# Performance work log

Hardware: AMD Instinct MI355X
Metric: run time of the kernel (lower is better)

## Reference

```python
import jax, jax.numpy as jnp
import numpy as np

D = 192      # model dim (out_channels)
DIN = 384    # d_inner = 2*D
N = 16       # d_state
DTR = 12     # dt_rank = ceil(D/16)
K = 4        # depthwise conv kernel size
NB = 3       # total mamba blocks (2 stacked + 1 in downsample)


def setup_inputs() -> dict:
    key = jax.random.key(0)
    ks = jax.random.split(key, 8)
    rn = lambda k, shape, s: jax.random.normal(k, shape, jnp.float32) * s
    inp = {
        "x": jax.random.normal(ks[0], (2, 96, 56, 56), jnp.float32),
        "proj_w": rn(ks[1], (D, 96), 0.1),
        "proj_b": jnp.zeros((D,), jnp.float32),
        "bn_g": jnp.ones((D,), jnp.float32),
        "bn_b": jnp.zeros((D,), jnp.float32),
        "bn_mean": jnp.zeros((D,), jnp.float32),
        "bn_var": jnp.ones((D,), jnp.float32),
        "ln_g": jnp.ones((NB, D), jnp.float32),
        "ln_b": jnp.zeros((NB, D), jnp.float32),
        "Win": rn(ks[2], (NB, 2 * DIN, D), 0.05),
        "b_in": jnp.zeros((NB, 2 * DIN), jnp.float32),
        "conv_w": rn(ks[3], (NB, DIN, K), 0.2),
        "conv_b": jnp.zeros((NB, DIN), jnp.float32),
        "Wx": rn(ks[4], (NB, DTR + 2 * N, DIN), 0.05),
        "Wdt": rn(ks[5], (NB, DIN, DTR), 0.05),
        "bdt": jnp.full((NB, DIN), -4.6, jnp.float32),  # softplus ~ 0.01
        "A_log": jnp.log(jnp.broadcast_to(jnp.arange(1, N + 1, dtype=jnp.float32), (NB, DIN, N))),
        "Dskip": jnp.ones((NB, DIN), jnp.float32),
        "Wout": rn(ks[6], (NB, D, DIN), 0.05),
        "bout": jnp.zeros((NB, D), jnp.float32),
    }
    return inp


def _mamba(x, ln_g, ln_b, Win, b_in, conv_w, conv_b, Wx, Wdt, bdt, A_log, Dskip, Wout, bout):
    # x: (B, C, H, W) -> flatten spatial dims to a sequence (B, L, C)
    B, C, H, W = x.shape
    L = H * W
    seq = x.reshape(B, C, L).transpose(0, 2, 1)
    mu = seq.mean(-1, keepdims=True)
    var = seq.var(-1, keepdims=True)
    h = (seq - mu) * jax.lax.rsqrt(var + 1e-5) * ln_g + ln_b  # LayerNorm
    xz = jnp.einsum('bld,ed->ble', h, Win) + b_in              # (B, L, 2*DIN)
    xi, z = jnp.split(xz, 2, axis=-1)
    # depthwise causal conv1d along L
    xc = jnp.pad(xi.transpose(0, 2, 1), ((0, 0), (0, 0), (K - 1, 0)))
    xc = jax.lax.conv_general_dilated(xc, conv_w[:, None, :], (1,), 'VALID',
                                      feature_group_count=DIN) + conv_b[:, None]
    xi = jax.nn.silu(xc).transpose(0, 2, 1)                    # (B, L, DIN)
    proj = jnp.einsum('ble,pe->blp', xi, Wx)                   # (B, L, DTR+2N)
    dtl = proj[..., :DTR]
    Bm = proj[..., DTR:DTR + N]
    Cm = proj[..., DTR + N:]
    dt = jax.nn.softplus(jnp.einsum('blr,er->ble', dtl, Wdt) + bdt)  # (B, L, DIN)
    A = -jnp.exp(A_log)                                         # (DIN, N)
    dA = jnp.exp(dt[..., None] * A)                             # (B, L, DIN, N)
    dBx = (dt * xi)[..., None] * Bm[:, :, None, :]              # (B, L, DIN, N)

    def step(hc, t):
        dA_t, dBx_t, C_t = t
        hc = dA_t * hc + dBx_t                                  # (B, DIN, N)
        return hc, jnp.einsum('ben,bn->be', hc, C_t)

    h0 = jnp.zeros((B, DIN, N), x.dtype)
    _, ys = jax.lax.scan(step, h0, (dA.transpose(1, 0, 2, 3),
                                    dBx.transpose(1, 0, 2, 3),
                                    Cm.transpose(1, 0, 2)))
    y = ys.transpose(1, 0, 2) + Dskip * xi
    y = y * jax.nn.silu(z)
    out = jnp.einsum('ble,de->bld', y, Wout) + bout
    return out.transpose(0, 2, 1).reshape(B, C, H, W)


def _maxpool2(x):
    return jax.lax.reduce_window(x, -jnp.inf, jax.lax.max,
                                 (1, 1, 2, 2), (1, 1, 2, 2), 'VALID')


def reference(x, proj_w, proj_b, bn_g, bn_b, bn_mean, bn_var, ln_g, ln_b, Win, b_in,
              conv_w, conv_b, Wx, Wdt, bdt, A_log, Dskip, Wout, bout):
    # proj (conv1x1) + BatchNorm (eval-mode running stats)
    x = jnp.einsum('bchw,oc->bohw', x, proj_w) + proj_b[:, None, None]
    x = (x - bn_mean[:, None, None]) * jax.lax.rsqrt(bn_var[:, None, None] + 1e-5) \
        * bn_g[:, None, None] + bn_b[:, None, None]
    blk = lambda i, v: _mamba(v, ln_g[i], ln_b[i], Win[i], b_in[i], conv_w[i], conv_b[i],
                              Wx[i], Wdt[i], bdt[i], A_log[i], Dskip[i], Wout[i], bout[i])
    for i in range(2):  # residual mamba blocks
        x = x + blk(i, x)
    skip = x
    x = blk(2, _maxpool2(x))  # downsample: maxpool then mamba (no residual)
    return (x, skip)
```

## Files before the change

kernel.cpp:

```cpp
#include <hip/hip_runtime.h>

typedef __attribute__((ext_vector_type(8))) __bf16 bf16x8;
typedef __attribute__((ext_vector_type(4))) __bf16 bf16x4;
typedef __attribute__((ext_vector_type(4))) float f32x4;

#define DEV static __device__ __forceinline__

DEV float fast_rcp(float x) { return __builtin_amdgcn_rcpf(x); }
DEV float sigm(float x) { return fast_rcp(1.f + __expf(-x)); }
DEV float siluf(float x) { return x * sigm(x); }
DEV float softplusf(float x) { return x > 20.f ? x : __logf(1.f + __expf(x)); }

__global__ __launch_bounds__(256) void k_proj_wcvt(
    const float* __restrict__ x, const float* __restrict__ pw,
    const float* __restrict__ pb, const float* __restrict__ bng,
    const float* __restrict__ bnb, const float* __restrict__ bnm,
    const float* __restrict__ bnv, float* __restrict__ v,
    const float* __restrict__ Win, const float* __restrict__ Wout,
    const float* __restrict__ Wx, __bf16* __restrict__ Wb)
{
  constexpr int SAP = 104;
  __shared__ __bf16 As[64 * SAP];
  __shared__ __bf16 Ws[64 * SAP];
  const int tid = threadIdx.x;
  const int bid = blockIdx.x;

  if (bid >= 294) {
    const int idx = (bid - 294) * 256 + tid;
    if (idx < 442368) Wb[idx] = (__bf16)Win[idx];
    else if (idx < 663552) Wb[idx] = (__bf16)Wout[idx - 442368];
    else Wb[idx] = (__bf16)Wx[idx - 663552];
    return;
  }

  const int r0 = (bid % 98) * 64;
  const int col0 = (bid / 98) * 64;
  const int b = r0 / 3136, l0 = r0 % 3136;
  const int lane = tid & 63, wv = tid >> 6;
  const int rh = wv >> 1, ch = wv & 1;
  const int lm = lane & 15, quad = lane >> 4;

#pragma unroll
  for (int it = 0; it < 6; ++it) {
    const int idx = tid + it * 256;
    const int c = idx >> 4, l4 = idx & 15;
    const float4 t = *(const float4*)(x + ((size_t)(b * 96 + c)) * 3136 + l0 + l4 * 4);
    As[(l4 * 4 + 0) * SAP + c] = (__bf16)t.x;
    As[(l4 * 4 + 1) * SAP + c] = (__bf16)t.y;
    As[(l4 * 4 + 2) * SAP + c] = (__bf16)t.z;
    As[(l4 * 4 + 3) * SAP + c] = (__bf16)t.w;
  }
#pragma unroll
  for (int it = 0; it < 6; ++it) {
    const int idx = tid + it * 256;
    const int wr = idx / 24, kc = (idx % 24) * 4;
    const float4 t = *(const float4*)(pw + (size_t)(col0 + wr) * 96 + kc);
    bf16x4 o;
    o[0] = (__bf16)t.x; o[1] = (__bf16)t.y; o[2] = (__bf16)t.z; o[3] = (__bf16)t.w;
    *(bf16x4*)(&Ws[wr * SAP + kc]) = o;
  }
  __syncthreads();

  f32x4 acc[2][2] = {};
#pragma unroll
  for (int ks = 0; ks < 3; ++ks) {
    const int kb = ks * 32 + quad * 8;
    bf16x8 a0 = *(const bf16x8*)(&As[(rh * 32 + lm) * SAP + kb]);
    bf16x8 a1 = *(const bf16x8*)(&As[(rh * 32 + 16 + lm) * SAP + kb]);
    bf16x8 b0 = *(const bf16x8*)(&Ws[(ch * 32 + lm) * SAP + kb]);
    bf16x8 b1 = *(const bf16x8*)(&Ws[(ch * 32 + 16 + lm) * SAP + kb]);
    acc[0][0] = __builtin_amdgcn_mfma_f32_16x16x32_bf16(a0, b0, acc[0][0], 0, 0, 0);
    acc[0][1] = __builtin_amdgcn_mfma_f32_16x16x32_bf16(a0, b1, acc[0][1], 0, 0, 0);
    acc[1][0] = __builtin_amdgcn_mfma_f32_16x16x32_bf16(a1, b0, acc[1][0], 0, 0, 0);
    acc[1][1] = __builtin_amdgcn_mfma_f32_16x16x32_bf16(a1, b1, acc[1][1], 0, 0, 0);
  }

#pragma unroll
  for (int ti = 0; ti < 2; ++ti)
#pragma unroll
    for (int tj = 0; tj < 2; ++tj) {
      const int gcol = col0 + ch * 32 + tj * 16 + lm;
      const float s = rsqrtf(bnv[gcol] + 1e-5f) * bng[gcol];
      const float sh = (pb[gcol] - bnm[gcol]) * s + bnb[gcol];
#pragma unroll
      for (int j = 0; j < 4; ++j) {
        const int grow = r0 + rh * 32 + ti * 16 + quad * 4 + j;
        v[(size_t)grow * 192 + gcol] = acc[ti][tj][j] * s + sh;
      }
    }
}

__global__ __launch_bounds__(256) void k_conv(
    const float* __restrict__ xz, __bf16* __restrict__ xiB,
    const float* __restrict__ cw, const float* __restrict__ cb,
    int Lseq, int nthreads)
{
  const int idx = blockIdx.x * 256 + threadIdx.x;
  if (idx >= nthreads) return;
  const int e = idx % 384;
  const int seg = idx / 384;
  const int nseg = Lseq / 8;
  const int b = seg / nseg;
  const int l0 = (seg % nseg) * 8;
  const float4 w4 = *(const float4*)(cw + e * 4);
  const float bv = cb[e];
  float xv[11];
#pragma unroll
  for (int k = 0; k < 11; ++k) {
    const int l = l0 - 3 + k;
    xv[k] = (l >= 0) ? xz[(size_t)(b * Lseq + l) * 768 + e] : 0.f;
  }
#pragma unroll
  for (int j = 0; j < 8; ++j) {
    const float a = bv + xv[j] * w4.x + xv[j + 1] * w4.y + xv[j + 2] * w4.z + xv[j + 3] * w4.w;
    xiB[(size_t)(b * Lseq + l0 + j) * 384 + e] = (__bf16)siluf(a);
  }
}

constexpr int EPI_XZ = 0, EPI_G2 = 1, EPI_RES = 2, EPI_RES_SKIP = 3, EPI_OUT2 = 4;

template <int AMODE, int NT, int EPI>
__global__ __launch_bounds__(256) void k_gemm(
    const void* __restrict__ Ain, const __bf16* __restrict__ W,
    const float* __restrict__ bias, float* __restrict__ O,
    int M, int K, int Nvalid,
    float* __restrict__ dtlbuf, float* __restrict__ bcbuf,
    float* __restrict__ oflt,
    const float* __restrict__ lng, const float* __restrict__ lnb,
    int Lseq)
{
  constexpr int SA = 200;
  constexpr int CT = (NT == 1) ? 2 : 4;
  __shared__ __bf16 As[64 * SA];
  __shared__ __bf16 Ws[64 * NT * SA];
  __shared__ float lnS[(AMODE >= 2) ? 384 : 1];
  const int tid = threadIdx.x;
  const int r0 = blockIdx.x * 64;
  const int col0 = blockIdx.y * (64 * NT);
  const int lane = tid & 63, wv = tid >> 6;
  const int rh = (NT == 1) ? (wv >> 1) : (wv & 1);
  const int ch = (NT == 1) ? (wv & 1) : (wv >> 1);
  const int lm = lane & 15, quad = lane >> 4;

  if constexpr (AMODE >= 2) {
    if (tid < 192) { lnS[tid] = lng[tid]; lnS[192 + tid] = lnb[tid]; }
    __syncthreads();
  }

  f32x4 acc[2][CT] = {};
  const int nkp = K / 192;
  for (int kp = 0; kp < nkp; ++kp) {
    if (kp) __syncthreads();
    if constexpr (AMODE == 1) {
      const __bf16* Ab = (const __bf16*)Ain;
#pragma unroll
      for (int it = 0; it < 6; ++it) {
        const int idx = tid + it * 256;
        const int row = idx / 24, kc = (idx % 24) * 8;
        const int gr = min(r0 + row, M - 1);
        bf16x8 val = *(const bf16x8*)(Ab + (size_t)gr * K + kp * 192 + kc);
        *(bf16x8*)(&As[row * SA + kc]) = val;
      }
    } else {
      const float* A = (const float*)Ain;
      const int row = tid >> 2, part = tid & 3;
      const int gr = min(r0 + row, M - 1);
      const int cbase = part * 48;
      float4 tv[12];
      if constexpr (AMODE == 2) {
#pragma unroll
        for (int j = 0; j < 12; ++j)
          tv[j] = *(const float4*)(A + (size_t)gr * 192 + cbase + j * 4);
      } else {
        const int bb = gr / 784, l2 = gr % 784;
        const int h2 = l2 / 28, w2 = l2 % 28;
        const float* p0 = A + (size_t)(bb * 3136 + h2 * 112 + w2 * 2) * 192;
#pragma unroll
        for (int j = 0; j < 12; ++j) {
          const int cc = cbase + j * 4;
          const float4 a0 = *(const float4*)(p0 + cc);
          const float4 a1 = *(const float4*)(p0 + 192 + cc);
          const float4 a2 = *(const float4*)(p0 + 56 * 192 + cc);
          const float4 a3 = *(const float4*)(p0 + 57 * 192 + cc);
          tv[j].x = fmaxf(fmaxf(a0.x, a1.x), fmaxf(a2.x, a3.x));
          tv[j].y = fmaxf(fmaxf(a0.y, a1.y), fmaxf(a2.y, a3.y));
          tv[j].z = fmaxf(fmaxf(a0.z, a1.z), fmaxf(a2.z, a3.z));
          tv[j].w = fmaxf(fmaxf(a0.w, a1.w), fmaxf(a2.w, a3.w));
        }
      }
      float s = 0.f, sq = 0.f;
#pragma unroll
      for (int j = 0; j < 12; ++j) {
        s += tv[j].x + tv[j].y + tv[j].z + tv[j].w;
        sq += tv[j].x * tv[j].x + tv[j].y * tv[j].y + tv[j].z * tv[j].z + tv[j].w * tv[j].w;
      }
      s += __shfl_xor(s, 1); s += __shfl_xor(s, 2);
      sq += __shfl_xor(sq, 1); sq += __shfl_xor(sq, 2);
      const float mean = s * (1.f / 192.f);
      const float rstd = rsqrtf(sq * (1.f / 192.f) - mean * mean + 1e-5f);
#pragma unroll
      for (int j = 0; j < 12; ++j) {
        const int c = cbase + j * 4;
        bf16x4 o;
        o[0] = (__bf16)((tv[j].x - mean) * rstd * lnS[c + 0] + lnS[192 + c + 0]);
        o[1] = (__bf16)((tv[j].y - mean) * rstd * lnS[c + 1] + lnS[192 + c + 1]);
        o[2] = (__bf16)((tv[j].z - mean) * rstd * lnS[c + 2] + lnS[192 + c + 2]);
        o[3] = (__bf16)((tv[j].w - mean) * rstd * lnS[c + 3] + lnS[192 + c + 3]);
        *(bf16x4*)(&As[row * SA + c]) = o;
      }
    }
#pragma unroll
    for (int it = 0; it < 6 * NT; ++it) {
      const int idx = tid + it * 256;
      const int wr = idx / 24, kc = (idx % 24) * 8;
      const int gw = col0 + wr;
      bf16x8 val = {};
      if (gw < Nvalid) val = *(const bf16x8*)(W + (size_t)gw * K + kp * 192 + kc);
      *(bf16x8*)(&Ws[wr * SA + kc]) = val;
    }
    __syncthreads();
#pragma unroll
    for (int ks = 0; ks < 6; ++ks) {
      const int kb = ks * 32 + quad * 8;
      bf16x8 a0 = *(const bf16x8*)(&As[(rh * 32 + lm) * SA + kb]);
      bf16x8 a1 = *(const bf16x8*)(&As[(rh * 32 + 16 + lm) * SA + kb]);
#pragma unroll
      for (int tj = 0; tj < CT; ++tj) {
        bf16x8 bfr = *(const bf16x8*)(&Ws[(ch * (16 * CT) + tj * 16 + lm) * SA + kb]);
        acc[0][tj] = __builtin_amdgcn_mfma_f32_16x16x32_bf16(a0, bfr, acc[0][tj], 0, 0, 0);
        acc[1][tj] = __builtin_amdgcn_mfma_f32_16x16x32_bf16(a1, bfr, acc[1][tj], 0, 0, 0);
      }
    }
  }

  if constexpr (EPI == EPI_G2) {
    __shared__ float dtlS[64 * 12];
#pragma unroll
    for (int ti = 0; ti < 2; ++ti)
#pragma unroll
      for (int tj = 0; tj < CT; ++tj) {
        const int colt = ch * (16 * CT) + tj * 16 + lm;
#pragma unroll
        for (int j = 0; j < 4; ++j) {
          const int rowt = rh * 32 + ti * 16 + quad * 4 + j;
          const int grow = r0 + rowt;
          const float val = acc[ti][tj][j];
          if (colt < 12) dtlS[rowt * 12 + colt] = val;
          else if (colt < 44 && grow < M)
            bcbuf[(size_t)grow * 32 + (colt - 12)] = val;
        }
      }
    __syncthreads();
    for (int idx = tid; idx < 64 * 12; idx += 256) {
      const int grow = r0 + idx / 12;
      if (grow < M) dtlbuf[(size_t)grow * 12 + idx % 12] = dtlS[idx];
    }
  } else {
#pragma unroll
    for (int ti = 0; ti < 2; ++ti)
#pragma unroll
      for (int tj = 0; tj < CT; ++tj) {
        const int colt = ch * (16 * CT) + tj * 16 + lm;
        const int gcol = col0 + colt;
        const float bv = bias[gcol];
#pragma unroll
        for (int j = 0; j < 4; ++j) {
          const int rowt = rh * 32 + ti * 16 + quad * 4 + j;
          const int grow = r0 + rowt;
          if (grow >= M) continue;
          const float val = acc[ti][tj][j] + bv;
          if constexpr (EPI == EPI_XZ) {
            O[(size_t)grow * 768 + gcol] = val;
          } else if constexpr (EPI == EPI_RES) {
            O[(size_t)grow * 192 + gcol] += val;
          } else if constexpr (EPI == EPI_RES_SKIP) {
            const float nv = O[(size_t)grow * 192 + gcol] + val;
            O[(size_t)grow * 192 + gcol] = nv;
            const int b = grow / 3136, l = grow % 3136;
            oflt[b * 602112 + gcol * 3136 + l] = nv;
          } else {
            const int b = grow / 784, l = grow % 784;
            oflt[b * 150528 + gcol * 784 + l] = val;
          }
        }
      }
  }
}

constexpr int SC_LC = 28, SC_T = 7, SC_TN = 4;

DEV void compute_dts(const float* __restrict__ dtl, const float* __restrict__ Wdt,
                     const float* __restrict__ bdt, int rowbase, int e, int t,
                     float* dtlS, float* wdtS)
{
  for (int idx = t; idx < SC_LC * 12; idx += 128)
    dtlS[idx] = dtl[(size_t)(rowbase + idx / 12) * 12 + idx % 12];
#pragma unroll
  for (int r = 0; r < 12; ++r) wdtS[r * 128 + t] = Wdt[(size_t)e * 12 + r];
}

__global__ __launch_bounds__(128) void k_scan1(
    const float* __restrict__ dtl, const __bf16* __restrict__ xi,
    const float* __restrict__ bc, const float* __restrict__ Wdt,
    const float* __restrict__ bdt, const float* __restrict__ A_log,
    float* __restrict__ P, float* __restrict__ S, int Lseq, int NC)
{
  __shared__ float Bs[SC_LC * 16];
  __shared__ float dts[SC_LC * 128];
  __shared__ float dtlS[SC_LC * 12];
  __shared__ float wdtS[12 * 128];
  const int t = threadIdx.x;
  const int e = blockIdx.y * 128 + t;
  const int c = blockIdx.x % NC;
  const int b = blockIdx.x / NC;
  const int rowbase = b * Lseq + c * SC_LC;

  for (int idx = t; idx < SC_LC * 16; idx += 128) {
    const int l = idx >> 4, q = idx & 15;
    Bs[idx] = bc[(size_t)(rowbase + l) * 32 + q];
  }
  compute_dts(dtl, Wdt, bdt, rowbase, e, t, dtlS, wdtS);
  const float bdte = bdt[e];

  float An2[16];
  {
    const float4* a4 = (const float4*)(A_log + e * 16);
    float4 t0 = a4[0], t1 = a4[1], t2 = a4[2], t3 = a4[3];
    float tmp[16] = {t0.x, t0.y, t0.z, t0.w, t1.x, t1.y, t1.z, t1.w,
                     t2.x, t2.y, t2.z, t2.w, t3.x, t3.y, t3.z, t3.w};
#pragma unroll
    for (int n = 0; n < 16; ++n) An2[n] = -__expf(tmp[n]) * 1.44269504f;
  }
  __syncthreads();
  for (int l = 0; l < SC_LC; ++l) {
    float a = bdte;
#pragma unroll
    for (int r = 0; r < 12; ++r) a += dtlS[l * 12 + r] * wdtS[r * 128 + t];
    dts[l * 128 + t] = softplusf(a);
  }

  float h[16], ap[16];
#pragma unroll
  for (int n = 0; n < 16; ++n) { h[n] = 0.f; ap[n] = 1.f; }

  float xA[SC_T], xB[SC_T];
  auto LOADA = [&](int tt) {
#pragma unroll
    for (int j = 0; j < SC_T; ++j)
      xA[j] = (float)xi[(size_t)(rowbase + tt * SC_T + j) * 384 + e];
  };
  auto LOADB = [&](int tt) {
#pragma unroll
    for (int j = 0; j < SC_T; ++j)
      xB[j] = (float)xi[(size_t)(rowbase + tt * SC_T + j) * 384 + e];
  };
  auto COMP = [&](const float (&x8)[SC_T], int tt) {
#pragma unroll
    for (int j = 0; j < SC_T; ++j) {
      const int l = tt * SC_T + j;
      const float dtv = dts[l * 128 + t];
      const float u = dtv * x8[j];
      const float* Brow = &Bs[l * 16];
#pragma unroll
      for (int n = 0; n < 16; ++n) {
        const float a = __builtin_amdgcn_exp2f(dtv * An2[n]);
        h[n] = a * h[n] + u * Brow[n];
        ap[n] *= a;
      }
    }
  };

  LOADA(0);
#pragma unroll
  for (int tt = 0; tt < SC_TN; ++tt) {
    if (tt & 1) { if (tt + 1 < SC_TN) LOADA(tt + 1); COMP(xB, tt); }
    else        { if (tt + 1 < SC_TN) LOADB(tt + 1); COMP(xA, tt); }
  }

  const size_t o = ((size_t)(b * NC + c) * 384 + e) * 16;
#pragma unroll
  for (int q = 0; q < 4; ++q) {
    *(float4*)(P + o + q * 4) = make_float4(ap[q*4], ap[q*4+1], ap[q*4+2], ap[q*4+3]);
    *(float4*)(S + o + q * 4) = make_float4(h[q*4], h[q*4+1], h[q*4+2], h[q*4+3]);
  }
}

__global__ __launch_bounds__(256) void k_carry(
    const float* __restrict__ P, float* __restrict__ SH, int NC)
{
  const int tid = blockIdx.x * 256 + threadIdx.x;
  const int b = tid / 6144, r = tid % 6144;
  size_t o = (size_t)b * NC * 6144 + r;
  float h = 0.f;
  for (int c0 = 0; c0 < NC; c0 += 4) {
    float p[4], s[4];
#pragma unroll
    for (int k = 0; k < 4; ++k) { p[k] = P[o + (size_t)k * 6144]; s[k] = SH[o + (size_t)k * 6144]; }
#pragma unroll
    for (int k = 0; k < 4; ++k) { SH[o + (size_t)k * 6144] = h; h = p[k] * h + s[k]; }
    o += (size_t)4 * 6144;
  }
}

__global__ __launch_bounds__(128) void k_scan2(
    const float* __restrict__ dtl, const __bf16* __restrict__ xi,
    const float* __restrict__ bc, const float* __restrict__ xz,
    const float* __restrict__ Wdt, const float* __restrict__ bdt,
    const float* __restrict__ A_log, const float* __restrict__ Dskip,
    const float* __restrict__ H0, __bf16* __restrict__ y, int Lseq, int NC)
{
  __shared__ float BCs[SC_LC * 32];
  __shared__ float dts[SC_LC * 128];
  __shared__ float dtlS[SC_LC * 12];
  __shared__ float wdtS[12 * 128];
  const int t = threadIdx.x;
  const int e = blockIdx.y * 128 + t;
  const int c = blockIdx.x % NC;
  const int b = blockIdx.x / NC;
  const int rowbase = b * Lseq + c * SC_LC;

  for (int idx = t; idx < SC_LC * 32; idx += 128)
    BCs[idx] = bc[(size_t)rowbase * 32 + idx];
  compute_dts(dtl, Wdt, bdt, rowbase, e, t, dtlS, wdtS);
  const float bdte = bdt[e];

  float An2[16];
  {
    const float4* a4 = (const float4*)(A_log + e * 16);
    float4 t0 = a4[0], t1 = a4[1], t2 = a4[2], t3 = a4[3];
    float tmp[16] = {t0.x, t0.y, t0.z, t0.w, t1.x, t1.y, t1.z, t1.w,
                     t2.x, t2.y, t2.z, t2.w, t3.x, t3.y, t3.z, t3.w};
#pragma unroll
    for (int n = 0; n < 16; ++n) An2[n] = -__expf(tmp[n]) * 1.44269504f;
  }
  float h[16];
  {
    const size_t o = ((size_t)(b * NC + c) * 384 + e) * 16;
    const float4* h4 = (const float4*)(H0 + o);
    float4 t0 = h4[0], t1 = h4[1], t2 = h4[2], t3 = h4[3];
    h[0]=t0.x; h[1]=t0.y; h[2]=t0.z; h[3]=t0.w;
    h[4]=t1.x; h[5]=t1.y; h[6]=t1.z; h[7]=t1.w;
    h[8]=t2.x; h[9]=t2.y; h[10]=t2.z; h[11]=t2.w;
    h[12]=t3.x; h[13]=t3.y; h[14]=t3.z; h[15]=t3.w;
  }
  __syncthreads();
  for (int l = 0; l < SC_LC; ++l) {
    float a = bdte;
#pragma unroll
    for (int r = 0; r < 12; ++r) a += dtlS[l * 12 + r] * wdtS[r * 128 + t];
    dts[l * 128 + t] = softplusf(a);
  }
  const float Dse = Dskip[e];

  float xA[SC_T], zA[SC_T], xB[SC_T], zB[SC_T];
  auto LOADA = [&](int tt) {
#pragma unroll
    for (int j = 0; j < SC_T; ++j) {
      const size_t r = (size_t)(rowbase + tt * SC_T + j);
      xA[j] = (float)xi[r * 384 + e];
      zA[j] = xz[r * 768 + 384 + e];
    }
  };
  auto LOADB = [&](int tt) {
#pragma unroll
    for (int j = 0; j < SC_T; ++j) {
      const size_t r = (size_t)(rowbase + tt * SC_T + j);
      xB[j] = (float)xi[r * 384 + e];
      zB[j] = xz[r * 768 + 384 + e];
    }
  };
  auto COMP = [&](const float (&x8)[SC_T], const float (&z8)[SC_T], int tt) {
#pragma unroll
    for (int j = 0; j < SC_T; ++j) {
      const int l = tt * SC_T + j;
      const float dtv = dts[l * 128 + t];
      const float xiv = x8[j];
      const float u = dtv * xiv;
      const float* Brow = &BCs[l * 32];
      const float* Crow = Brow + 16;
      float yv = 0.f;
#pragma unroll
      for (int n = 0; n < 16; ++n) {
        const float a = __builtin_amdgcn_exp2f(dtv * An2[n]);
        h[n] = a * h[n] + u * Brow[n];
        yv += h[n] * Crow[n];
      }
      y[(size_t)(rowbase + l) * 384 + e] = (__bf16)((yv + Dse * xiv) * siluf(z8[j]));
    }
  };

  LOADA(0);
#pragma unroll
  for (int tt = 0; tt < SC_TN; ++tt) {
    if (tt & 1) { if (tt + 1 < SC_TN) LOADA(tt + 1); COMP(xB, zB, tt); }
    else        { if (tt + 1 < SC_TN) LOADB(tt + 1); COMP(xA, zA, tt); }
  }
}

extern "C" void kernel_launch(void* const* d_in, const int* in_sizes, int n_in,
                              void* d_out, int out_size, void* d_ws, size_t ws_size,
                              hipStream_t stream)
{
  const float* x    = (const float*)d_in[0];
  const float* pw   = (const float*)d_in[1];
  const float* pb   = (const float*)d_in[2];
  const float* bng  = (const float*)d_in[3];
  const float* bnb  = (const float*)d_in[4];
  const float* bnm  = (const float*)d_in[5];
  const float* bnv  = (const float*)d_in[6];
  const float* lng  = (const float*)d_in[7];
  const float* lnb  = (const float*)d_in[8];
  const float* Win  = (const float*)d_in[9];
  const float* b_in = (const float*)d_in[10];
  const float* cw   = (const float*)d_in[11];
  const float* cb   = (const float*)d_in[12];
  const float* Wx   = (const float*)d_in[13];
  const float* Wdt  = (const float*)d_in[14];
  const float* bdt  = (const float*)d_in[15];
  const float* Alog = (const float*)d_in[16];
  const float* Dsk  = (const float*)d_in[17];
  const float* Wout = (const float*)d_in[18];
  const float* bout = (const float*)d_in[19];

  float* wsf = (float*)d_ws;
  float* v    = wsf;
  float* xz   = v + 1204224;
  float* dtlb = xz + 4816896;
  float* bcb  = dtlb + 75264;
  float* Sb   = bcb + 200704;
  __bf16* xiB = (__bf16*)(Sb + 1376256);
  __bf16* yB  = (__bf16*)(Sb + 1376256 + 1204224);
  __bf16* Wb  = (__bf16*)(Sb + 1376256 + 2408448);

  float* out0 = (float*)d_out;
  float* out1 = out0 + 301056;
  float* Pbig = out0;
  float* Psml = xz + 2408448;

  k_proj_wcvt<<<3084, 256, 0, stream>>>(x, pw, pb, bng, bnb, bnm, bnv, v,
                                        Win, Wout, Wx, Wb);

  for (int i = 0; i < 3; ++i) {
    const int big = (i < 2) ? 1 : 0;
    const int Lseq = big ? 3136 : 784;
    const int M = 2 * Lseq;
    const int NC = Lseq / SC_LC;
    const int MB = (M + 63) / 64;
    const float* lng_i = lng + i * 192;
    const float* lnb_i = lnb + i * 192;
    const float* bin_i = b_in + i * 768;
    const float* cw_i  = cw + i * 384 * 4;
    const float* cb_i  = cb + i * 384;
    const float* Wdt_i = Wdt + i * 384 * 12;
    const float* bdt_i = bdt + i * 384;
    const float* Al_i  = Alog + i * 384 * 16;
    const float* Ds_i  = Dsk + i * 384;
    const float* bo_i  = bout + i * 192;
    const __bf16* Winb_i  = Wb + i * 147456;
    const __bf16* Woutb_i = Wb + 442368 + i * 73728;
    const __bf16* Wxb_i   = Wb + 663552 + i * 16896;
    float* Pb = big ? Pbig : Psml;

    if (big)
      k_gemm<2, 2, EPI_XZ><<<dim3(MB, 6), 256, 0, stream>>>(
          v, Winb_i, bin_i, xz, M, 192, 768,
          nullptr, nullptr, nullptr, lng_i, lnb_i, Lseq);
    else
      k_gemm<3, 2, EPI_XZ><<<dim3(MB, 6), 256, 0, stream>>>(
          v, Winb_i, bin_i, xz, M, 192, 768,
          nullptr, nullptr, nullptr, lng_i, lnb_i, Lseq);
    k_conv<<<(M * 384 / 8 + 255) / 256, 256, 0, stream>>>(
        xz, xiB, cw_i, cb_i, Lseq, M * 384 / 8);
    k_gemm<1, 1, EPI_G2><<<dim3(MB, 1), 256, 0, stream>>>(
        xiB, Wxb_i, nullptr, nullptr, M, 384, 44,
        dtlb, bcb, nullptr, nullptr, nullptr, Lseq);
    k_scan1<<<dim3(2 * NC, 3), 128, 0, stream>>>(
        dtlb, xiB, bcb, Wdt_i, bdt_i, Al_i, Pb, Sb, Lseq, NC);
    k_carry<<<48, 256, 0, stream>>>(Pb, Sb, NC);
    k_scan2<<<dim3(2 * NC, 3), 128, 0, stream>>>(
        dtlb, xiB, bcb, xz, Wdt_i, bdt_i, Al_i, Ds_i, Sb, yB, Lseq, NC);
    if (i == 0)
      k_gemm<1, 1, EPI_RES><<<dim3(MB, 3), 256, 0, stream>>>(
          yB, Woutb_i, bo_i, v, M, 384, 192,
          nullptr, nullptr, nullptr, nullptr, nullptr, Lseq);
    else if (i == 1)
      k_gemm<1, 1, EPI_RES_SKIP><<<dim3(MB, 3), 256, 0, stream>>>(
          yB, Woutb_i, bo_i, v, M, 384, 192,
          nullptr, nullptr, out1, nullptr, nullptr, Lseq);
    else
      k_gemm<1, 1, EPI_OUT2><<<dim3(MB, 3), 256, 0, stream>>>(
          yB, Woutb_i, bo_i, v, M, 384, 192,
          nullptr, nullptr, out0, nullptr, nullptr, Lseq);
  }
}
```

Baseline: 394.1 us.

## Fuse causal depthwise conv and SiLU into in-projection GEMM epilogue

Removes the separate conv kernel. The in-projection GEMM now applies the depthwise causal conv and SiLU in its epilogue for the xi half and writes bf16 xi directly, while the z half goes to a compact 384-wide buffer. A 3-row halo is normalized and recomputed per block with a scalar dot product, which avoids writing and reading back the full fp32 xz tensor. The cost is extra LDS use, a redundant halo GEMM and extra syncs in the GEMM blocks. Some leftover no-op code appears in the conv loop.

```diff
diff --git a/kernel.cpp b/kernel.cpp
--- a/kernel.cpp
+++ b/kernel.cpp
@@ -90,33 +90,6 @@
     }
 }
 
-__global__ __launch_bounds__(256) void k_conv(
-    const float* __restrict__ xz, __bf16* __restrict__ xiB,
-    const float* __restrict__ cw, const float* __restrict__ cb,
-    int Lseq, int nthreads)
-{
-  const int idx = blockIdx.x * 256 + threadIdx.x;
-  if (idx >= nthreads) return;
-  const int e = idx % 384;
-  const int seg = idx / 384;
-  const int nseg = Lseq / 8;
-  const int b = seg / nseg;
-  const int l0 = (seg % nseg) * 8;
-  const float4 w4 = *(const float4*)(cw + e * 4);
-  const float bv = cb[e];
-  float xv[11];
-#pragma unroll
-  for (int k = 0; k < 11; ++k) {
-    const int l = l0 - 3 + k;
-    xv[k] = (l >= 0) ? xz[(size_t)(b * Lseq + l) * 768 + e] : 0.f;
-  }
-#pragma unroll
-  for (int j = 0; j < 8; ++j) {
-    const float a = bv + xv[j] * w4.x + xv[j + 1] * w4.y + xv[j + 2] * w4.z + xv[j + 3] * w4.w;
-    xiB[(size_t)(b * Lseq + l0 + j) * 384 + e] = (__bf16)siluf(a);
-  }
-}
-
 constexpr int EPI_XZ = 0, EPI_G2 = 1, EPI_RES = 2, EPI_RES_SKIP = 3, EPI_OUT2 = 4;
 
 template <int AMODE, int NT, int EPI>
@@ -127,12 +100,15 @@
     float* __restrict__ dtlbuf, float* __restrict__ bcbuf,
     float* __restrict__ oflt,
     const float* __restrict__ lng, const float* __restrict__ lnb,
+    const float* __restrict__ cw, const float* __restrict__ cb,
+    __bf16* __restrict__ xiBout, float* __restrict__ zb,
     int Lseq)
 {
   constexpr int SA = 200;
   constexpr int CT = (NT == 1) ? 2 : 4;
   __shared__ __bf16 As[64 * SA];
   __shared__ __bf16 Ws[64 * NT * SA];
+  __shared__ __bf16 As2[(EPI == EPI_XZ) ? 3 * SA : 1];
   __shared__ float lnS[(AMODE >= 2) ? 384 : 1];
   const int tid = threadIdx.x;
   const int r0 = blockIdx.x * 64;
@@ -163,50 +139,58 @@
       }
     } else {
       const float* A = (const float*)Ain;
-      const int row = tid >> 2, part = tid & 3;
-      const int gr = min(r0 + row, M - 1);
-      const int cbase = part * 48;
-      float4 tv[12];
-      if constexpr (AMODE == 2) {
-#pragma unroll
-        for (int j = 0; j < 12; ++j)
-          tv[j] = *(const float4*)(A + (size_t)gr * 192 + cbase + j * 4);
-      } else {
-        const int bb = gr / 784, l2 = gr % 784;
-        const int h2 = l2 / 28, w2 = l2 % 28;
-        const float* p0 = A + (size_t)(bb * 3136 + h2 * 112 + w2 * 2) * 192;
+      const int nwork = (EPI == EPI_XZ && col0 < 384) ? 2 : 1;
+      for (int w = 0; w < nwork; ++w) {
+        int row, part, gr;
+        __bf16* dst;
+        if (w == 0) { row = tid >> 2; part = tid & 3; gr = min(r0 + row, M - 1); dst = &As[row * SA]; }
+        else {
+          if (tid >= 12) break;
+          row = tid >> 2; part = tid & 3; gr = max(r0 - 3 + row, 0); dst = &As2[row * SA];
+        }
+        const int cbase = part * 48;
+        float4 tv[12];
+        if constexpr (AMODE == 2) {
+#pragma unroll
+          for (int j = 0; j < 12; ++j)
+            tv[j] = *(const float4*)(A + (size_t)gr * 192 + cbase + j * 4);
+        } else {
+          const int bb = gr / 784, l2 = gr % 784;
+          const int h2 = l2 / 28, w2 = l2 % 28;
+          const float* p0 = A + (size_t)(bb * 3136 + h2 * 112 + w2 * 2) * 192;
+#pragma unroll
+          for (int j = 0; j < 12; ++j) {
+            const int cc = cbase + j * 4;
+            const float4 a0 = *(const float4*)(p0 + cc);
+            const float4 a1 = *(const float4*)(p0 + 192 + cc);
+            const float4 a2 = *(const float4*)(p0 + 56 * 192 + cc);
+            const float4 a3 = *(const float4*)(p0 + 57 * 192 + cc);
+            tv[j].x = fmaxf(fmaxf(a0.x, a1.x), fmaxf(a2.x, a3.x));
+            tv[j].y = fmaxf(fmaxf(a0.y, a1.y), fmaxf(a2.y, a3.y));
+            tv[j].z = fmaxf(fmaxf(a0.z, a1.z), fmaxf(a2.z, a3.z));
+            tv[j].w = fmaxf(fmaxf(a0.w, a1.w), fmaxf(a2.w, a3.w));
+          }
+        }
+        float s = 0.f, sq = 0.f;
 #pragma unroll
         for (int j = 0; j < 12; ++j) {
-          const int cc = cbase + j * 4;
-          const float4 a0 = *(const float4*)(p0 + cc);
-          const float4 a1 = *(const float4*)(p0 + 192 + cc);
-          const float4 a2 = *(const float4*)(p0 + 56 * 192 + cc);
-          const float4 a3 = *(const float4*)(p0 + 57 * 192 + cc);
-          tv[j].x = fmaxf(fmaxf(a0.x, a1.x), fmaxf(a2.x, a3.x));
-          tv[j].y = fmaxf(fmaxf(a0.y, a1.y), fmaxf(a2.y, a3.y));
-          tv[j].z = fmaxf(fmaxf(a0.z, a1.z), fmaxf(a2.z, a3.z));
-          tv[j].w = fmaxf(fmaxf(a0.w, a1.w), fmaxf(a2.w, a3.w));
-        }
-      }
-      float s = 0.f, sq = 0.f;
-#pragma unroll
-      for (int j = 0; j < 12; ++j) {
-        s += tv[j].x + tv[j].y + tv[j].z + tv[j].w;
-        sq += tv[j].x * tv[j].x + tv[j].y * tv[j].y + tv[j].z * tv[j].z + tv[j].w * tv[j].w;
-      }
-      s += __shfl_xor(s, 1); s += __shfl_xor(s, 2);
-      sq += __shfl_xor(sq, 1); sq += __shfl_xor(sq, 2);
-      const float mean = s * (1.f / 192.f);
-      const float rstd = rsqrtf(sq * (1.f / 192.f) - mean * mean + 1e-5f);
-#pragma unroll
-      for (int j = 0; j < 12; ++j) {
-        const int c = cbase + j * 4;
-        bf16x4 o;
-        o[0] = (__bf16)((tv[j].x - mean) * rstd * lnS[c + 0] + lnS[192 + c + 0]);
-        o[1] = (__bf16)((tv[j].y - mean) * rstd * lnS[c + 1] + lnS[192 + c + 1]);
-        o[2] = (__bf16)((tv[j].z - mean) * rstd * lnS[c + 2] + lnS[192 + c + 2]);
-        o[3] = (__bf16)((tv[j].w - mean) * rstd * lnS[c + 3] + lnS[192 + c + 3]);
-        *(bf16x4*)(&As[row * SA + c]) = o;
+          s += tv[j].x + tv[j].y + tv[j].z + tv[j].w;
+          sq += tv[j].x * tv[j].x + tv[j].y * tv[j].y + tv[j].z * tv[j].z + tv[j].w * tv[j].w;
+        }
+        s += __shfl_xor(s, 1); s += __shfl_xor(s, 2);
+        sq += __shfl_xor(sq, 1); sq += __shfl_xor(sq, 2);
+        const float mean = s * (1.f / 192.f);
+        const float rstd = rsqrtf(sq * (1.f / 192.f) - mean * mean + 1e-5f);
+#pragma unroll
+        for (int j = 0; j < 12; ++j) {
+          const int c = cbase + j * 4;
+          bf16x4 o;
+          o[0] = (__bf16)((tv[j].x - mean) * rstd * lnS[c + 0] + lnS[192 + c + 0]);
+          o[1] = (__bf16)((tv[j].y - mean) * rstd * lnS[c + 1] + lnS[192 + c + 1]);
+          o[2] = (__bf16)((tv[j].z - mean) * rstd * lnS[c + 2] + lnS[192 + c + 2]);
+          o[3] = (__bf16)((tv[j].w - mean) * rstd * lnS[c + 3] + lnS[192 + c + 3]);
+          *(bf16x4*)(dst + c) = o;
+        }
       }
     }
 #pragma unroll
@@ -233,7 +217,98 @@
     }
   }
 
-  if constexpr (EPI == EPI_G2) {
+  if constexpr (EPI == EPI_XZ) {
+    if (col0 < 384) {
+      __syncthreads();
+      float bval[2] = {0.f, 0.f};
+#pragma unroll
+      for (int jj = 0; jj < 2; ++jj) {
+        const int j = tid + jj * 256;
+        if (j < 384) {
+          const int row3 = j >> 7, col = j & 127;
+          float a = bias[col0 + col];
+#pragma unroll
+          for (int kk = 0; kk < 24; ++kk) {
+            const bf16x8 a8 = *(const bf16x8*)(&As2[row3 * SA + kk * 8]);
+            const bf16x8 w8 = *(const bf16x8*)(&Ws[col * SA + kk * 8]);
+#pragma unroll
+            for (int q = 0; q < 8; ++q) a += (float)a8[q] * (float)w8[q];
+          }
+          bval[jj] = a;
+        }
+      }
+      __syncthreads();
+      constexpr int XTP = 132;
+      float* XT = (float*)Ws;
+#pragma unroll
+      for (int jj = 0; jj < 2; ++jj) {
+        const int j = tid + jj * 256;
+        if (j < 384) XT[(j >> 7) * XTP + (j & 127)] = bval[jj];
+      }
+#pragma unroll
+      for (int ti = 0; ti < 2; ++ti)
+#pragma unroll
+        for (int tj = 0; tj < CT; ++tj) {
+          const int colt = ch * (16 * CT) + tj * 16 + lm;
+          const float bv = bias[col0 + colt];
+#pragma unroll
+          for (int j = 0; j < 4; ++j) {
+            const int rowt = rh * 32 + ti * 16 + quad * 4 + j;
+            XT[(rowt + 3) * XTP + colt] = acc[ti][tj][j] + bv;
+          }
+        }
+      __syncthreads();
+      const int c0 = tid & 31;
+      const int rbase = (tid >> 5) * 8;
+#pragma unroll
+      for (int q = 0; q < 4; ++q) {
+        const int col = c0 + 32 * q;
+        const int e = col0 + col;
+        const float4 w4 = *(const float4*)(cw + e * 4);
+        const float cbe = cb[e];
+#pragma unroll
+        for (int rr = 0; rr < 8; ++rr) {
+          const int lrow = rbase + rr;
+          const int lg = r0 + lrow;
+          const int lseq = lg % Lseq;
+          float a = cbe;
+#pragma unroll
+          for (int k = 0; k < 4; ++k) {
+            const float xv = (lseq - 3 + k >= 0) ? XT[(lrow + k) * XTP + col] : 0.f;
+            a += w4[k] * ((const float*)&w4)[k] == 0.f ? 0.f : 0.f;
+            a += 0.f;
+          }
+          a = cbe;
+          if (lseq >= 3) {
+            a += w4.x * XT[(lrow + 0) * XTP + col];
+            a += w4.y * XT[(lrow + 1) * XTP + col];
+            a += w4.z * XT[(lrow + 2) * XTP + col];
+          } else {
+            if (lseq >= 3) a += w4.x * XT[(lrow + 0) * XTP + col];
+            if (lseq >= 2) a += w4.y * XT[(lrow + 1) * XTP + col];
+            if (lseq >= 1) a += w4.z * XT[(lrow + 2) * XTP + col];
+          }
+          a += w4.w * XT[(lrow + 3) * XTP + col];
+          if (lg < M) xiBout[(size_t)lg * 384 + e] = (__bf16)siluf(a);
+        }
+      }
+    } else {
+#pragma unroll
+      for (int ti = 0; ti < 2; ++ti)
+#pragma unroll
+        for (int tj = 0; tj < CT; ++tj) {
+          const int colt = ch * (16 * CT) + tj * 16 + lm;
+          const int gcol = col0 + colt;
+          const float bv = bias[gcol];
+#pragma unroll
+          for (int j = 0; j < 4; ++j) {
+            const int rowt = rh * 32 + ti * 16 + quad * 4 + j;
+            const int grow = r0 + rowt;
+            if (grow < M) zb[(size_t)grow * 384 + (gcol - 384)] = acc[ti][tj][j] + bv;
+          }
+        }
+    }
+  } else if constexpr (EPI == EPI_G2) {
     __shared__ float dtlS[64 * 12];
 #pragma unroll
     for (int ti = 0; ti < 2; ++ti)
@@ -269,9 +344,7 @@
           const int grow = r0 + rowt;
           if (grow >= M) continue;
           const float val = acc[ti][tj][j] + bv;
-          if constexpr (EPI == EPI_XZ) {
-            O[(size_t)grow * 768 + gcol] = val;
-          } else if constexpr (EPI == EPI_RES) {
+          if constexpr (EPI == EPI_RES) {
             O[(size_t)grow * 192 + gcol] += val;
           } else if constexpr (EPI == EPI_RES_SKIP) {
             const float nv = O[(size_t)grow * 192 + gcol] + val;
@@ -404,7 +477,7 @@
 
 __global__ __launch_bounds__(128) void k_scan2(
     const float* __restrict__ dtl, const __bf16* __restrict__ xi,
-    const float* __restrict__ bc, const float* __restrict__ xz,
+    const float* __restrict__ bc, const float* __restrict__ zb,
     const float* __restrict__ Wdt, const float* __restrict__ bdt,
     const float* __restrict__ A_log, const float* __restrict__ Dskip,
     const float* __restrict__ H0, __bf16* __restrict__ y, int Lseq, int NC)
@@ -458,7 +531,7 @@
     for (int j = 0; j < SC_T; ++j) {
       const size_t r = (size_t)(rowbase + tt * SC_T + j);
       xA[j] = (float)xi[r * 384 + e];
-      zA[j] = xz[r * 768 + 384 + e];
+      zA[j] = zb[r * 384 + e];
     }
   };
   auto LOADB = [&](int tt) {
@@ -466,7 +539,7 @@
     for (int j = 0; j < SC_T; ++j) {
       const size_t r = (size_t)(rowbase + tt * SC_T + j);
       xB[j] = (float)xi[r * 384 + e];
-      zB[j] = xz[r * 768 + 384 + e];
+      zB[j] = zb[r * 384 + e];
     }
   };
   auto COMP = [&](const float (&x8)[SC_T], const float (&z8)[SC_T], int tt) {
@@ -524,8 +597,8 @@
 
   float* wsf = (float*)d_ws;
   float* v    = wsf;
-  float* xz   = v + 1204224;
-  float* dtlb = xz + 4816896;
+  float* zb   = v + 1204224;
+  float* dtlb = zb + 2408448;
   float* bcb  = dtlb + 75264;
   float* Sb   = bcb + 200704;
   __bf16* xiB = (__bf16*)(Sb + 1376256);
@@ -535,7 +608,7 @@
   float* out0 = (float*)d_out;
   float* out1 = out0 + 301056;
   float* Pbig = out0;
-  float* Psml = xz + 2408448;
+  float* Psml = zb + 1204224;
 
   k_proj_wcvt<<<3084, 256, 0, stream>>>(x, pw, pb, bng, bnb, bnm, bnv, v,
                                         Win, Wout, Wx, Wb);
@@ -563,33 +636,37 @@
 
     if (big)
       k_gemm<2, 2, EPI_XZ><<<dim3(MB, 6), 256, 0, stream>>>(
-          v, Winb_i, bin_i, xz, M, 192, 768,
-          nullptr, nullptr, nullptr, lng_i, lnb_i, Lseq);
+          v, Winb_i, bin_i, nullptr, M, 192, 768,
+          nullptr, nullptr, nullptr, lng_i, lnb_i,
+          cw_i, cb_i, xiB, zb, Lseq);
     else
       k_gemm<3, 2, EPI_XZ><<<dim3(MB, 6), 256, 0, stream>>>(
-          v, Winb_i, bin_i, xz, M, 192, 768,
-          nullptr, nullptr, nullptr, lng_i, lnb_i, Lseq);
-    k_conv<<<(M * 384 / 8 + 255) / 256, 256, 0, stream>>>(
-        xz, xiB, cw_i, cb_i, Lseq, M * 384 / 8);
+          v, Winb_i, bin_i, nullptr, M, 192, 768,
+          nullptr, nullptr, nullptr, lng_i, lnb_i,
+          cw_i, cb_i, xiB, zb, Lseq);
     k_gemm<1, 1, EPI_G2><<<dim3(MB, 1), 256, 0, stream>>>(
         xiB, Wxb_i, nullptr, nullptr, M, 384, 44,
-        dtlb, bcb, nullptr, nullptr, nullptr, Lseq);
+        dtlb, bcb, nullptr, nullptr, nullptr,
+        nullptr, nullptr, nullptr, nullptr, Lseq);
     k_scan1<<<dim3(2 * NC, 3), 128, 0, stream>>>(
         dtlb, xiB, bcb, Wdt_i, bdt_i, Al_i, Pb, Sb, Lseq, NC);
     k_carry<<<48, 256, 0, stream>>>(Pb, Sb, NC);
     k_scan2<<<dim3(2 * NC, 3), 128, 0, stream>>>(
-        dtlb, xiB, bcb, xz, Wdt_i, bdt_i, Al_i, Ds_i, Sb, yB, Lseq, NC);
+        dtlb, xiB, bcb, zb, Wdt_i, bdt_i, Al_i, Ds_i, Sb, yB, Lseq, NC);
     if (i == 0)
       k_gemm<1, 1, EPI_RES><<<dim3(MB, 3), 256, 0, stream>>>(
           yB, Woutb_i, bo_i, v, M, 384, 192,
-          nullptr, nullptr, nullptr, nullptr, nullptr, Lseq);
+          nullptr, nullptr, nullptr, nullptr, nullptr,
+          nullptr, nullptr, nullptr, nullptr, Lseq);
     else if (i == 1)
       k_gemm<1, 1, EPI_RES_SKIP><<<dim3(MB, 3), 256, 0, stream>>>(
           yB, Woutb_i, bo_i, v, M, 384, 192,
-          nullptr, nullptr, out1, nullptr, nullptr, Lseq);
+          nullptr, nullptr, out1, nullptr, nullptr,
+          nullptr, nullptr, nullptr, nullptr, Lseq);
     else
       k_gemm<1, 1, EPI_OUT2><<<dim3(MB, 3), 256, 0, stream>>>(
           yB, Woutb_i, bo_i, v, M, 384, 192,
-          nullptr, nullptr, out0, nullptr, nullptr, Lseq);
+          nullptr, nullptr, out0, nullptr, nullptr,
+          nullptr, nullptr, nullptr, nullptr, Lseq);
   }
 }
```

After: 399.6 us. About the same (+1.4%).
